# Kernel tuning notes

Measured on AMD Instinct MI355X. Metric: run time of the kernel, lower is better.

The kernel has to match this reference:

```python
import jax, jax.numpy as jnp
import numpy as np

EMB = 256
IN_CH = 256
CTX_D = 128


def setup_inputs() -> dict:
    key = jax.random.key(0)
    ks = jax.random.split(key, 12)
    b, c, h, w = 16, IN_CH, 48, 48
    seq = 2048
    s = 0.02
    return {
        "x": jax.random.normal(ks[0], (b, c, h, w), jnp.float32),
        "context": jax.random.normal(ks[1], (b, seq, CTX_D), jnp.float32),
        "pad_mask": jax.random.bernoulli(ks[2], 0.1, (b, h * w, seq)),
        "W_in": jax.random.normal(ks[3], (EMB, IN_CH), jnp.float32) * s,   # 1x1 conv weight
        "b_in": jnp.zeros((EMB,), jnp.float32),
        "Wq": jax.random.normal(ks[4], (EMB, EMB), jnp.float32) * s,
        "bq": jnp.zeros((EMB,), jnp.float32),
        "Wk": jax.random.normal(ks[5], (EMB, CTX_D), jnp.float32) * s,
        "bk": jnp.zeros((EMB,), jnp.float32),
        "Wv": jax.random.normal(ks[6], (EMB, CTX_D), jnp.float32) * s,
        "bv": jnp.zeros((EMB,), jnp.float32),
        "W_out": jax.random.normal(ks[7], (IN_CH, EMB), jnp.float32) * s,  # 1x1 conv weight
        "b_out": jnp.zeros((IN_CH,), jnp.float32),
    }


def reference(x, context, pad_mask, W_in, b_in, Wq, bq, Wk, bk, Wv, bv, W_out, b_out):
    b, c, h, w = x.shape
    scale = EMB ** (-0.5)
    # proj_in: 1x1 conv == channel matmul; then b c h w -> b (h w) c
    xt = jnp.einsum('bchw,ec->behw', x, W_in) + b_in[None, :, None, None]
    xt = xt.reshape(b, EMB, h * w).transpose(0, 2, 1)          # [b, hw, emb]
    Q = xt @ Wq.T + bq                                          # [b, hw, emb]
    K = context @ Wk.T + bk                                     # [b, seq, emb]
    V = context @ Wv.T + bv                                     # [b, seq, emb]
    att = jnp.einsum('bid,bjd->bij', Q, K) * scale              # [b, hw, seq]
    att = jnp.where(pad_mask, jnp.float32(-1e9), att)
    att = jax.nn.softmax(att, axis=-1)
    out = jnp.einsum('bij,bjd->bid', att, V)                    # [b, hw, emb]
    out = out.transpose(0, 2, 1).reshape(b, EMB, h, w)
    out = jnp.einsum('behw,ce->bchw', out, W_out) + b_out[None, :, None, None]
    return out, att
```

## Files before the change

### kernel.cpp

```cpp
#include <hip/hip_runtime.h>

typedef unsigned short u16;
typedef unsigned int   u32;
typedef __attribute__((ext_vector_type(8))) __bf16 bf16x8;
typedef __attribute__((ext_vector_type(4))) float  f32x4;

#define BB   16
#define CH   256
#define HW   2304
#define SEQ  2048
#define EMB  256
#define CTXD 128
#define OUT0 9437184

#define MFMA(a,b,c) __builtin_amdgcn_mfma_f32_16x16x32_bf16(a,b,c,0,0,0)

__device__ __forceinline__ u16 f2bf(float f){
  u32 u = __builtin_bit_cast(u32, f);
  u += 0x7fffu + ((u >> 16) & 1u);
  return (u16)(u >> 16);
}
__device__ __forceinline__ float bf2f(u32 us){ return __builtin_bit_cast(float, us << 16); }

__device__ __forceinline__ bf16x8 ld16(const u16* p){
  uint4 q = *reinterpret_cast<const uint4*>(p);
  return __builtin_bit_cast(bf16x8, q);
}
__device__ __forceinline__ bf16x8 mk8(float a0,float a1,float a2,float a3,
                                      float a4,float a5,float a6,float a7){
  uint4 q;
  q.x = (u32)f2bf(a0) | ((u32)f2bf(a1) << 16);
  q.y = (u32)f2bf(a2) | ((u32)f2bf(a3) << 16);
  q.z = (u32)f2bf(a4) | ((u32)f2bf(a5) << 16);
  q.w = (u32)f2bf(a6) | ((u32)f2bf(a7) << 16);
  return __builtin_bit_cast(bf16x8, q);
}
__device__ __forceinline__ void gload16(const u16* g, u16* l){
  __builtin_amdgcn_global_load_lds(
      (const __attribute__((address_space(1))) unsigned int*)(const void*)g,
      (__attribute__((address_space(3))) unsigned int*)(void*)l, 16, 0, 0);
}

__global__ __launch_bounds__(256) void k_prep(
    const float* __restrict__ Wq, const float* __restrict__ W_in,
    const float* __restrict__ b_in, const float* __restrict__ bq,
    const float* __restrict__ Wk, const float* __restrict__ Wv,
    const float* __restrict__ Wout,
    u16* __restrict__ WqinBf, u16* __restrict__ WkBf, u16* __restrict__ WvBf,
    u16* __restrict__ WoutBf, float* __restrict__ bq_eff)
{
  int blk = blockIdx.x, t = threadIdx.x;
  const float SC = 0.0625f;
  if (blk < 256) {
    int e = blk, c = t;
    float s = 0.f;
    for (int f = 0; f < 256; f++) s += Wq[e*256+f] * W_in[f*256+c];
    WqinBf[e*256+c] = f2bf(s * SC);
    if (t == 0) {
      float bb = bq[e];
      for (int f = 0; f < 256; f++) bb += Wq[e*256+f] * b_in[f];
      bq_eff[e] = bb * SC;
    }
  } else {
    u32 flat = (u32)(blk - 256) * 256 + t;
    for (u32 idx = flat; idx < 131072u; idx += 16384u) {
      if (idx < 32768u)       WkBf[idx]          = f2bf(Wk[idx]);
      else if (idx < 65536u)  WvBf[idx - 32768u] = f2bf(Wv[idx - 32768u]);
      else                    WoutBf[idx - 65536u] = f2bf(Wout[idx - 65536u]);
    }
  }
}

__global__ __launch_bounds__(256) void k_qproj(
    const float* __restrict__ x, const u16* __restrict__ WqinBf,
    const float* __restrict__ bq_eff, u16* __restrict__ Qbf)
{
  int b = blockIdx.y, ibase = blockIdx.x * 64;
  int t = threadIdx.x, wv = t >> 6, lane = t & 63, g4 = lane >> 4, r16 = lane & 15;
  int e0 = wv * 64;
  f32x4 acc[4][4] = {};
  #pragma unroll 2
  for (int kk = 0; kk < 8; kk++) {
    bf16x8 a[4];
    #pragma unroll
    for (int m = 0; m < 4; m++)
      a[m] = ld16(WqinBf + (size_t)(e0 + m*16 + r16) * 256 + kk*32 + g4*8);
    bf16x8 bb[4];
    #pragma unroll
    for (int n = 0; n < 4; n++) {
      const float* xp = x + ((size_t)b*CH + kk*32 + g4*8) * HW + ibase + n*16 + r16;
      bb[n] = mk8(xp[0], xp[HW], xp[2*HW], xp[3*HW], xp[4*HW], xp[5*HW], xp[6*HW], xp[7*HW]);
    }
    #pragma unroll
    for (int m = 0; m < 4; m++)
      #pragma unroll
      for (int n = 0; n < 4; n++)
        acc[m][n] = MFMA(a[m], bb[n], acc[m][n]);
  }
  #pragma unroll
  for (int m = 0; m < 4; m++) {
    int e = e0 + m*16 + g4*4;
    float b0 = bq_eff[e], b1 = bq_eff[e+1], b2 = bq_eff[e+2], b3 = bq_eff[e+3];
    #pragma unroll
    for (int n = 0; n < 4; n++) {
      int i = ibase + n*16 + r16;
      u32 lo = (u32)f2bf(acc[m][n][0] + b0) | ((u32)f2bf(acc[m][n][1] + b1) << 16);
      u32 hi = (u32)f2bf(acc[m][n][2] + b2) | ((u32)f2bf(acc[m][n][3] + b3) << 16);
      *(uint2*)(Qbf + ((size_t)b*HW + i) * EMB + e) = make_uint2(lo, hi);
    }
  }
}

__global__ __launch_bounds__(512) void k_kvproj(
    const float* __restrict__ ctx, const u16* __restrict__ WkBf, const u16* __restrict__ WvBf,
    const float* __restrict__ bk, const float* __restrict__ bv,
    u16* __restrict__ Kbf, u16* __restrict__ Vtb)
{
  int b = blockIdx.y, sbase = blockIdx.x * 64;
  int t = threadIdx.x, wv = t >> 6, lane = t & 63, g4 = lane >> 4, r16 = lane & 15;
  bool isV = wv >= 4;
  int e0 = (wv & 3) * 64;
  const u16* Wsel = isV ? WvBf : WkBf;
  f32x4 acc[4][4] = {};
  #pragma unroll
  for (int kk = 0; kk < 4; kk++) {
    bf16x8 a[4];
    #pragma unroll
    for (int m = 0; m < 4; m++)
      a[m] = ld16(Wsel + (size_t)(e0 + m*16 + r16) * 128 + kk*32 + g4*8);
    bf16x8 bb[4];
    #pragma unroll
    for (int n = 0; n < 4; n++) {
      const float* cp = ctx + ((size_t)b*SEQ + sbase + n*16 + r16) * CTXD + kk*32 + g4*8;
      float4 lo = *(const float4*)cp;
      float4 hi = *(const float4*)(cp + 4);
      bb[n] = mk8(lo.x, lo.y, lo.z, lo.w, hi.x, hi.y, hi.z, hi.w);
    }
    #pragma unroll
    for (int m = 0; m < 4; m++)
      #pragma unroll
      for (int n = 0; n < 4; n++)
        acc[m][n] = MFMA(a[m], bb[n], acc[m][n]);
  }
  if (!isV) {
    #pragma unroll
    for (int m = 0; m < 4; m++) {
      int e = e0 + m*16 + g4*4;
      float b0 = bk[e], b1 = bk[e+1], b2 = bk[e+2], b3 = bk[e+3];
      #pragma unroll
      for (int n = 0; n < 4; n++) {
        int s = sbase + n*16 + r16;
        u32 lo = (u32)f2bf(acc[m][n][0] + b0) | ((u32)f2bf(acc[m][n][1] + b1) << 16);
        u32 hi = (u32)f2bf(acc[m][n][2] + b2) | ((u32)f2bf(acc[m][n][3] + b3) << 16);
        *(uint2*)(Kbf + ((size_t)b*SEQ + s) * EMB + e) = make_uint2(lo, hi);
      }
    }
  } else {
    #pragma unroll
    for (int m = 0; m < 4; m++) {
      #pragma unroll
      for (int r = 0; r < 4; r++) {
        int e = e0 + m*16 + g4*4 + r;
        float bvv = bv[e];
        #pragma unroll
        for (int n = 0; n < 4; n++) {
          int s = sbase + n*16 + r16;
          Vtb[((size_t)b*EMB + e) * SEQ + s] = f2bf(acc[m][n][r] + bvv);
        }
      }
    }
  }
}

__global__ __launch_bounds__(512, 4) void k_qk(
    const u16* __restrict__ Qbf, const u16* __restrict__ Kbf,
    const int* __restrict__ mask, float* __restrict__ dout,
    float* __restrict__ gpart)
{
  __shared__ u16 lsA[128*64];
  __shared__ u16 lsB[128*64];
  __shared__ float red[4][128];

  int bid = blockIdx.x;
  int work = (bid & 7) * 576 + (bid >> 3);
  int b = work / 288, rem = work % 288;
  int mt = rem / 16, jt = rem % 16;
  int mbase = mt * 128, jbase = jt * 128;
  size_t bH = (size_t)b * HW, bS = (size_t)b * SEQ;

  int t = threadIdx.x, wv = t >> 6, lane = t & 63, g4 = lane >> 4, r16 = lane & 15;
  int wr = wv >> 2, wc = wv & 3;

  int mreg[4][2][4];
  {
    const int* mp = mask + (bH + mbase + wr*64 + g4*4) * SEQ + jbase + wc*32 + r16;
    #pragma unroll
    for (int m = 0; m < 4; m++)
      #pragma unroll
      for (int n = 0; n < 2; n++)
        #pragma unroll
        for (int r = 0; r < 4; r++)
          mreg[m][n][r] = mp[(size_t)(m*16 + r) * SEQ + n*16];
  }

  int srow = t >> 3, sc8 = (t & 7) * 8;
  const u16* qsrc = Qbf + (bH + mbase + srow) * 256 + sc8;
  const u16* ksrc = Kbf + (bS + jbase + srow) * 256 + sc8;
  u16* ldstA = lsA + (size_t)t * 8;
  u16* ldstB = lsB + (size_t)t * 8;

  f32x4 acc[4][2] = {};
  #pragma unroll 1
  for (int ks = 0; ks < 4; ks++) {
    gload16(qsrc + ks*64,             ldstA);
    gload16(qsrc + ks*64 + 64*256,    ldstA + 4096);
    gload16(ksrc + ks*64,             ldstB);
    gload16(ksrc + ks*64 + 64*256,    ldstB + 4096);
    __syncthreads();
    #pragma unroll
    for (int kk = 0; kk < 2; kk++) {
      bf16x8 af[4], bf[2];
      #pragma unroll
      for (int m = 0; m < 4; m++)
        af[m] = ld16(lsA + (size_t)(wr*64 + m*16 + r16) * 64 + kk*32 + g4*8);
      #pragma unroll
      for (int n = 0; n < 2; n++)
        bf[n] = ld16(lsB + (size_t)(wc*32 + n*16 + r16) * 64 + kk*32 + g4*8);
      #pragma unroll
      for (int m = 0; m < 4; m++)
        #pragma unroll
        for (int n = 0; n < 2; n++)
          acc[m][n] = MFMA(af[m], bf[n], acc[m][n]);
    }
    __syncthreads();
  }

  u16* Ebase = (u16*)(dout + OUT0);
  float part[4][4] = {};
  #pragma unroll
  for (int m = 0; m < 4; m++)
    #pragma unroll
    for (int n = 0; n < 2; n++)
      #pragma unroll
      for (int r = 0; r < 4; r++) {
        float e = mreg[m][n][r] ? 0.f : __expf(acc[m][n][r]);
        part[m][r] += e;
        int i = wr*64 + m*16 + g4*4 + r;
        int j = jbase + wc*32 + n*16 + r16;
        Ebase[(bH + mbase + i) * 4096 + 2048 + j] = f2bf(e);
      }
  #pragma unroll
  for (int m = 0; m < 4; m++)
    #pragma unroll
    for (int r = 0; r < 4; r++) {
      float v = part[m][r];
      v += __shfl_xor(v, 1); v += __shfl_xor(v, 2);
      v += __shfl_xor(v, 4); v += __shfl_xor(v, 8);
      if (r16 == 0) red[wc][wr*64 + m*16 + g4*4 + r] = v;
    }
  __syncthreads();
  if (t < 128) {
    float tot = red[0][t] + red[1][t] + red[2][t] + red[3][t];
    gpart[(bH + mbase + t) * 16 + jt] = tot;
  }
}

__global__ __launch_bounds__(512, 4) void k_pv(
    const u16* __restrict__ Vtb, const float* __restrict__ gpart,
    float* __restrict__ dout, u16* __restrict__ Obf)
{
  __shared__ u16 lsE[64*64];
  __shared__ u16 lsV[256*64];
  __shared__ float invl[64];

  int bid = blockIdx.x;
  int work = (bid & 7) * 72 + (bid >> 3);
  int b = work / 36, mt = work % 36;
  int mbase = mt * 64;
  size_t bH = (size_t)b * HW;

  int t = threadIdx.x, wv = t >> 6, lane = t & 63, g4 = lane >> 4, r16 = lane & 15;

  if (t < 64) {
    const float4* pp = (const float4*)(gpart + (bH + mbase + t) * 16);
    float4 p0 = pp[0], p1 = pp[1], p2 = pp[2], p3 = pp[3];
    float s = p0.x+p0.y+p0.z+p0.w + p1.x+p1.y+p1.z+p1.w
            + p2.x+p2.y+p2.z+p2.w + p3.x+p3.y+p3.z+p3.w;
    invl[t] = 1.f / s;
  }

  const u16* Ebase = (const u16*)(dout + OUT0);
  float* attb = dout + OUT0;
  int srow = t >> 3, sc8 = (t & 7) * 8;
  const u16* esrc = Ebase + (bH + mbase + srow) * 4096 + 2048 + sc8;
  u16* ldstE = lsE + (size_t)t * 8;

  f32x4 acc[4][2] = {};
  #pragma unroll 1
  for (int c = 0; c < 32; c++) {
    int kb = c * 64;
    gload16(esrc + kb, ldstE);
    #pragma unroll
    for (int it = 0; it < 4; it++) {
      int idx = it*512 + t;
      gload16(Vtb + ((size_t)b*EMB + (idx >> 3)) * SEQ + kb + (idx & 7)*8,
              lsV + (size_t)idx * 8);
    }
    __syncthreads();
    #pragma unroll
    for (int kk = 0; kk < 2; kk++) {
      bf16x8 aE[4], bV[2];
      #pragma unroll
      for (int m = 0; m < 4; m++)
        aE[m] = ld16(lsE + (size_t)(m*16 + r16) * 64 + kk*32 + g4*8);
      #pragma unroll
      for (int n = 0; n < 2; n++)
        bV[n] = ld16(lsV + (size_t)(wv*32 + n*16 + r16) * 64 + kk*32 + g4*8);
      #pragma unroll
      for (int m = 0; m < 4; m++)
        #pragma unroll
        for (int n = 0; n < 2; n++)
          acc[m][n] = MFMA(aE[m], bV[n], acc[m][n]);
    }
    {
      float iv = invl[srow];
      const u16* ep = lsE + (size_t)srow * 64 + sc8;
      float* ar = attb + (bH + mbase + srow) * 2048 + kb + sc8;
      float4 o0, o1;
      o0.x = bf2f(ep[0]) * iv; o0.y = bf2f(ep[1]) * iv;
      o0.z = bf2f(ep[2]) * iv; o0.w = bf2f(ep[3]) * iv;
      o1.x = bf2f(ep[4]) * iv; o1.y = bf2f(ep[5]) * iv;
      o1.z = bf2f(ep[6]) * iv; o1.w = bf2f(ep[7]) * iv;
      *(float4*)ar = o0;
      *(float4*)(ar + 4) = o1;
    }
    __syncthreads();
  }

  #pragma unroll
  for (int m = 0; m < 4; m++)
    #pragma unroll
    for (int n = 0; n < 2; n++)
      #pragma unroll
      for (int r = 0; r < 4; r++) {
        int i = m*16 + g4*4 + r;
        int e = wv*32 + n*16 + r16;
        Obf[(bH + mbase + i) * 256 + e] = f2bf(acc[m][n][r] * invl[i]);
      }
}

__global__ __launch_bounds__(256) void k_outproj(
    const u16* __restrict__ Obf, const u16* __restrict__ WoutBf,
    const float* __restrict__ bout, float* __restrict__ out)
{
  int b = blockIdx.y, ibase = blockIdx.x * 64;
  int t = threadIdx.x, wv = t >> 6, lane = t & 63, g4 = lane >> 4, r16 = lane & 15;
  int c0 = wv * 64;
  f32x4 acc[4][4] = {};
  #pragma unroll 2
  for (int kk = 0; kk < 8; kk++) {
    bf16x8 a[4];
    #pragma unroll
    for (int m = 0; m < 4; m++)
      a[m] = ld16(WoutBf + (size_t)(c0 + m*16 + r16) * 256 + kk*32 + g4*8);
    bf16x8 bb[4];
    #pragma unroll
    for (int n = 0; n < 4; n++)
      bb[n] = ld16(Obf + ((size_t)b*HW + ibase + n*16 + r16) * EMB + kk*32 + g4*8);
    #pragma unroll
    for (int m = 0; m < 4; m++)
      #pragma unroll
      for (int n = 0; n < 4; n++)
        acc[m][n] = MFMA(a[m], bb[n], acc[m][n]);
  }
  #pragma unroll
  for (int m = 0; m < 4; m++) {
    #pragma unroll
    for (int r = 0; r < 4; r++) {
      int c = c0 + m*16 + g4*4 + r;
      float bo = bout[c];
      #pragma unroll
      for (int n = 0; n < 4; n++) {
        int i = ibase + n*16 + r16;
        out[((size_t)b*CH + c) * HW + i] = acc[m][n][r] + bo;
      }
    }
  }
}

extern "C" void kernel_launch(void* const* d_in, const int* in_sizes, int n_in,
                              void* d_out, int out_size, void* d_ws, size_t ws_size,
                              hipStream_t stream)
{
  const float* x    = (const float*)d_in[0];
  const float* ctx  = (const float*)d_in[1];
  const int*   mask = (const int*)  d_in[2];
  const float* W_in = (const float*)d_in[3];
  const float* b_in = (const float*)d_in[4];
  const float* Wq   = (const float*)d_in[5];
  const float* bq   = (const float*)d_in[6];
  const float* Wk   = (const float*)d_in[7];
  const float* bk   = (const float*)d_in[8];
  const float* Wv   = (const float*)d_in[9];
  const float* bv   = (const float*)d_in[10];
  const float* Wout = (const float*)d_in[11];
  const float* bout = (const float*)d_in[12];
  float* out = (float*)d_out;

  char* ws = (char*)d_ws;
  size_t off = 0;
  auto alloc = [&](size_t bytes) -> void* {
    void* p = ws + off;
    off += (bytes + 255) & ~(size_t)255;
    return p;
  };
  u16*   WqinBf = (u16*)  alloc(256*256*2);
  u16*   WkBf   = (u16*)  alloc(256*128*2);
  u16*   WvBf   = (u16*)  alloc(256*128*2);
  u16*   WoutBf = (u16*)  alloc(256*256*2);
  float* bq_eff = (float*)alloc(256*4);
  float* gpart  = (float*)alloc((size_t)BB*HW*16*4);
  u16*   Qbf    = (u16*)  alloc((size_t)BB*HW*EMB*2);
  u16*   Kbf    = (u16*)  alloc((size_t)BB*SEQ*EMB*2);
  u16*   Vtb    = (u16*)  alloc((size_t)BB*EMB*SEQ*2);
  if (off > ws_size) return;

  k_prep<<<dim3(320), dim3(256), 0, stream>>>(Wq, W_in, b_in, bq, Wk, Wv, Wout,
                                              WqinBf, WkBf, WvBf, WoutBf, bq_eff);
  k_qproj<<<dim3(36, 16), dim3(256), 0, stream>>>(x, WqinBf, bq_eff, Qbf);
  k_kvproj<<<dim3(32, 16), dim3(512), 0, stream>>>(ctx, WkBf, WvBf, bk, bv, Kbf, Vtb);
  k_qk<<<dim3(4608), dim3(512), 0, stream>>>(Qbf, Kbf, mask, out, gpart);
  k_pv<<<dim3(576), dim3(512), 0, stream>>>(Vtb, gpart, out, Qbf );
  k_outproj<<<dim3(36, 16), dim3(256), 0, stream>>>(Qbf , WoutBf, bout, out);
}
```

Measured before the change: 471.0 us.

## XOR-swizzle LDS tiles in QK and PV, retile PV to 32-row blocks

```diff
diff --git a/kernel.cpp b/kernel.cpp
--- a/kernel.cpp
+++ b/kernel.cpp
@@ -23,6 +23,10 @@
 __device__ __forceinline__ float bf2f(u32 us){ return __builtin_bit_cast(float, us << 16); }
 
 __device__ __forceinline__ bf16x8 ld16(const u16* p){
+  uint4 q = *reinterpret_cast<const uint4*>(p);
+  return __builtin_bit_cast(bf16x8, q);
+}
+__device__ __forceinline__ bf16x8 ld16c(const char* p){
   uint4 q = *reinterpret_cast<const uint4*>(p);
   return __builtin_bit_cast(bf16x8, q);
 }
@@ -54,13 +58,17 @@
   if (blk < 256) {
     int e = blk, c = t;
     float s = 0.f;
+    #pragma unroll 8
     for (int f = 0; f < 256; f++) s += Wq[e*256+f] * W_in[f*256+c];
     WqinBf[e*256+c] = f2bf(s * SC);
-    if (t == 0) {
-      float bb = bq[e];
-      for (int f = 0; f < 256; f++) bb += Wq[e*256+f] * b_in[f];
-      bq_eff[e] = bb * SC;
-    }
+    __shared__ float rb[4];
+    float pb = Wq[e*256+t] * b_in[t];
+    pb += __shfl_xor(pb, 1);  pb += __shfl_xor(pb, 2);
+    pb += __shfl_xor(pb, 4);  pb += __shfl_xor(pb, 8);
+    pb += __shfl_xor(pb, 16); pb += __shfl_xor(pb, 32);
+    if ((t & 63) == 0) rb[t >> 6] = pb;
+    __syncthreads();
+    if (t == 0) bq_eff[e] = (rb[0]+rb[1]+rb[2]+rb[3] + bq[e]) * SC;
   } else {
     u32 flat = (u32)(blk - 256) * 256 + t;
     for (u32 idx = flat; idx < 131072u; idx += 16384u) {
@@ -188,7 +196,7 @@
   int mbase = mt * 128, jbase = jt * 128;
   size_t bH = (size_t)b * HW, bS = (size_t)b * SEQ;
 
-  int t = threadIdx.x, wv = t >> 6, lane = t & 63, g4 = lane >> 4, r16 = lane & 15;
+  int t = threadIdx.x, lane = t & 63, wv = t >> 6, g4 = lane >> 4, r16 = lane & 15;
   int wr = wv >> 2, wc = wv & 3;
 
   int mreg[4][2][4];
@@ -203,29 +211,39 @@
           mreg[m][n][r] = mp[(size_t)(m*16 + r) * SEQ + n*16];
   }
 
-  int srow = t >> 3, sc8 = (t & 7) * 8;
-  const u16* qsrc = Qbf + (bH + mbase + srow) * 256 + sc8;
-  const u16* ksrc = Kbf + (bS + jbase + srow) * 256 + sc8;
-  u16* ldstA = lsA + (size_t)t * 8;
-  u16* ldstB = lsB + (size_t)t * 8;
+  int i0 = t, i1 = t + 512;
+  int r0 = i0 >> 3, c0 = (i0 & 7) ^ (r0 & 7);
+  int r1 = i1 >> 3, c1 = (i1 & 7) ^ (r1 & 7);
+  const u16* qs0 = Qbf + (bH + mbase + r0) * 256 + c0*8;
+  const u16* qs1 = Qbf + (bH + mbase + r1) * 256 + c1*8;
+  const u16* ks0 = Kbf + (bS + jbase + r0) * 256 + c0*8;
+  const u16* ks1 = Kbf + (bS + jbase + r1) * 256 + c1*8;
+  u16 *dA0 = lsA + i0*8, *dA1 = lsA + i1*8, *dB0 = lsB + i0*8, *dB1 = lsB + i1*8;
+
+  const char* lA = (const char*)lsA;
+  const char* lB = (const char*)lsB;
 
   f32x4 acc[4][2] = {};
   #pragma unroll 1
   for (int ks = 0; ks < 4; ks++) {
-    gload16(qsrc + ks*64,             ldstA);
-    gload16(qsrc + ks*64 + 64*256,    ldstA + 4096);
-    gload16(ksrc + ks*64,             ldstB);
-    gload16(ksrc + ks*64 + 64*256,    ldstB + 4096);
+    gload16(qs0 + ks*64, dA0);
+    gload16(qs1 + ks*64, dA1);
+    gload16(ks0 + ks*64, dB0);
+    gload16(ks1 + ks*64, dB1);
     __syncthreads();
     #pragma unroll
     for (int kk = 0; kk < 2; kk++) {
       bf16x8 af[4], bf[2];
       #pragma unroll
-      for (int m = 0; m < 4; m++)
-        af[m] = ld16(lsA + (size_t)(wr*64 + m*16 + r16) * 64 + kk*32 + g4*8);
-      #pragma unroll
-      for (int n = 0; n < 2; n++)
-        bf[n] = ld16(lsB + (size_t)(wc*32 + n*16 + r16) * 64 + kk*32 + g4*8);
+      for (int m = 0; m < 4; m++) {
+        int row = wr*64 + m*16 + r16;
+        af[m] = ld16c(lA + row*128 + (((kk<<2)|g4) ^ (row&7))*16);
+      }
+      #pragma unroll
+      for (int n = 0; n < 2; n++) {
+        int row = wc*32 + n*16 + r16;
+        bf[n] = ld16c(lB + row*128 + (((kk<<2)|g4) ^ (row&7))*16);
+      }
       #pragma unroll
       for (int m = 0; m < 4; m++)
         #pragma unroll
@@ -265,23 +283,23 @@
   }
 }
 
-__global__ __launch_bounds__(512, 4) void k_pv(
+__global__ __launch_bounds__(256, 4) void k_pv(
     const u16* __restrict__ Vtb, const float* __restrict__ gpart,
     float* __restrict__ dout, u16* __restrict__ Obf)
 {
-  __shared__ u16 lsE[64*64];
+  __shared__ u16 lsE[32*64];
   __shared__ u16 lsV[256*64];
-  __shared__ float invl[64];
+  __shared__ float invl[32];
 
   int bid = blockIdx.x;
-  int work = (bid & 7) * 72 + (bid >> 3);
-  int b = work / 36, mt = work % 36;
-  int mbase = mt * 64;
+  int work = (bid & 7) * 144 + (bid >> 3);
+  int b = work / 72, mt = work % 72;
+  int mbase = mt * 32;
   size_t bH = (size_t)b * HW;
 
-  int t = threadIdx.x, wv = t >> 6, lane = t & 63, g4 = lane >> 4, r16 = lane & 15;
-
-  if (t < 64) {
+  int t = threadIdx.x, lane = t & 63, wv = t >> 6, g4 = lane >> 4, r16 = lane & 15;
+
+  if (t < 32) {
     const float4* pp = (const float4*)(gpart + (bH + mbase + t) * 16);
     float4 p0 = pp[0], p1 = pp[1], p2 = pp[2], p3 = pp[3];
     float s = p0.x+p0.y+p0.z+p0.w + p1.x+p1.y+p1.z+p1.w
@@ -291,60 +309,72 @@
 
   const u16* Ebase = (const u16*)(dout + OUT0);
   float* attb = dout + OUT0;
-  int srow = t >> 3, sc8 = (t & 7) * 8;
-  const u16* esrc = Ebase + (bH + mbase + srow) * 4096 + 2048 + sc8;
-  u16* ldstE = lsE + (size_t)t * 8;
-
-  f32x4 acc[4][2] = {};
+  int rE = t >> 3, cE = (t & 7) ^ (rE & 7);
+  const u16* esrc = Ebase + (bH + mbase + rE) * 4096 + 2048 + cE*8;
+  u16* dE = lsE + t*8;
+  int rV[8], cV[8];
+  #pragma unroll
+  for (int i = 0; i < 8; i++) {
+    int idx = i*256 + t;
+    rV[i] = idx >> 3;
+    cV[i] = (idx & 7) ^ (rV[i] & 7);
+  }
+  const char* lE = (const char*)lsE;
+  const char* lV = (const char*)lsV;
+  int srow = t >> 3;
+  u32 sxor = (u32)((t & 7) ^ (srow & 7)) * 16;
+  float* arow = attb + (bH + mbase + srow) * 2048 + (t & 7) * 8;
+
+  f32x4 acc[2][4] = {};
   #pragma unroll 1
   for (int c = 0; c < 32; c++) {
     int kb = c * 64;
-    gload16(esrc + kb, ldstE);
-    #pragma unroll
-    for (int it = 0; it < 4; it++) {
-      int idx = it*512 + t;
-      gload16(Vtb + ((size_t)b*EMB + (idx >> 3)) * SEQ + kb + (idx & 7)*8,
-              lsV + (size_t)idx * 8);
-    }
+    gload16(esrc + kb, dE);
+    #pragma unroll
+    for (int i = 0; i < 8; i++)
+      gload16(Vtb + ((size_t)b*EMB + rV[i]) * SEQ + kb + cV[i]*8, lsV + (i*256 + t)*8);
     __syncthreads();
     #pragma unroll
     for (int kk = 0; kk < 2; kk++) {
-      bf16x8 aE[4], bV[2];
-      #pragma unroll
-      for (int m = 0; m < 4; m++)
-        aE[m] = ld16(lsE + (size_t)(m*16 + r16) * 64 + kk*32 + g4*8);
-      #pragma unroll
-      for (int n = 0; n < 2; n++)
-        bV[n] = ld16(lsV + (size_t)(wv*32 + n*16 + r16) * 64 + kk*32 + g4*8);
-      #pragma unroll
-      for (int m = 0; m < 4; m++)
+      bf16x8 aE[2], bV[4];
+      #pragma unroll
+      for (int m = 0; m < 2; m++) {
+        int row = m*16 + r16;
+        aE[m] = ld16c(lE + row*128 + (((kk<<2)|g4) ^ (row&7))*16);
+      }
+      #pragma unroll
+      for (int n = 0; n < 4; n++) {
+        int row = wv*64 + n*16 + r16;
+        bV[n] = ld16c(lV + row*128 + (((kk<<2)|g4) ^ (row&7))*16);
+      }
+      #pragma unroll
+      for (int m = 0; m < 2; m++)
         #pragma unroll
-        for (int n = 0; n < 2; n++)
+        for (int n = 0; n < 4; n++)
           acc[m][n] = MFMA(aE[m], bV[n], acc[m][n]);
     }
     {
       float iv = invl[srow];
-      const u16* ep = lsE + (size_t)srow * 64 + sc8;
-      float* ar = attb + (bH + mbase + srow) * 2048 + kb + sc8;
+      const u16* ep = (const u16*)(lE + srow*128 + sxor);
       float4 o0, o1;
       o0.x = bf2f(ep[0]) * iv; o0.y = bf2f(ep[1]) * iv;
       o0.z = bf2f(ep[2]) * iv; o0.w = bf2f(ep[3]) * iv;
       o1.x = bf2f(ep[4]) * iv; o1.y = bf2f(ep[5]) * iv;
       o1.z = bf2f(ep[6]) * iv; o1.w = bf2f(ep[7]) * iv;
-      *(float4*)ar = o0;
-      *(float4*)(ar + 4) = o1;
+      *(float4*)(arow + kb) = o0;
+      *(float4*)(arow + kb + 4) = o1;
     }
     __syncthreads();
   }
 
   #pragma unroll
-  for (int m = 0; m < 4; m++)
-    #pragma unroll
-    for (int n = 0; n < 2; n++)
+  for (int m = 0; m < 2; m++)
+    #pragma unroll
+    for (int n = 0; n < 4; n++)
       #pragma unroll
       for (int r = 0; r < 4; r++) {
         int i = m*16 + g4*4 + r;
-        int e = wv*32 + n*16 + r16;
+        int e = wv*64 + n*16 + r16;
         Obf[(bH + mbase + i) * 256 + e] = f2bf(acc[m][n][r] * invl[i]);
       }
 }
@@ -430,6 +460,6 @@
   k_qproj<<<dim3(36, 16), dim3(256), 0, stream>>>(x, WqinBf, bq_eff, Qbf);
   k_kvproj<<<dim3(32, 16), dim3(512), 0, stream>>>(ctx, WkBf, WvBf, bk, bv, Kbf, Vtb);
   k_qk<<<dim3(4608), dim3(512), 0, stream>>>(Qbf, Kbf, mask, out, gpart);
-  k_pv<<<dim3(576), dim3(512), 0, stream>>>(Vtb, gpart, out, Qbf );
+  k_pv<<<dim3(1152), dim3(256), 0, stream>>>(Vtb, gpart, out, Qbf );
   k_outproj<<<dim3(36, 16), dim3(256), 0, stream>>>(Qbf , WoutBf, bout, out);
 }
```

Measured after the change: 430.7 us. 8.6% less time.
